# Kernel optimization log

Hardware: AMD Instinct MI355X
Metric: run time of the kernel (lower is better)

## Reference

```python
import jax, jax.numpy as jnp
import numpy as np

EMBED_DIM = 256
NUM_CLASSES = 10


def setup_inputs() -> dict:
    key = jax.random.key(0)
    k1, k2, k3, k4 = jax.random.split(key, 4)
    x = jax.random.normal(k1, (64, 196, 768), dtype=jnp.float32)
    ag_w = jax.random.normal(k2, (EMBED_DIM, 768), dtype=jnp.float32)
    ag_b = jax.random.normal(k3, (EMBED_DIM,), dtype=jnp.float32)
    lm_w = jax.random.normal(k4, (EMBED_DIM * NUM_CLASSES, 768), dtype=jnp.float32)
    return {"x": x, "ag_w": ag_w, "ag_b": ag_b, "lm_w": lm_w}


def reference(x, ag_w, ag_b, lm_w):
    # x: (B, HW, D); ag_w: (E, D); ag_b: (E,); lm_w: (E*C, D)
    B, HW, D = x.shape
    E, C = EMBED_DIM, NUM_CLASSES
    # frozen arrangement generator -> binary sign pattern (B, HW, E)
    sign_patterns = (jnp.einsum('bhd,ed->bhe', x, ag_w) + ag_b > 0).astype(x.dtype)
    # linear map: (B, HW, E*C) -> (B, HW, E, C)
    z = jnp.einsum('bhd,pd->bhp', x, lm_w).reshape(B, HW, E, C)
    # masked reduction over HW and embed dims
    preds = jnp.einsum('bhp,bhpc->bc', sign_patterns, z) / HW
    return preds / E
```

## Files before the change

### kernel.cpp

```cpp
#include <hip/hip_runtime.h>

#define B_    64
#define HW_   196
#define HWP_  224
#define D_    768
#define E_    256
#define C_    10
#define MP_   (B_*HWP_)
#define K3K_  (E_*D_)
#define K3NB_ 192

typedef __bf16 bf16x8 __attribute__((ext_vector_type(8)));
typedef __bf16 bf16x4 __attribute__((ext_vector_type(4)));
typedef float  f32x4  __attribute__((ext_vector_type(4)));

__device__ __forceinline__ void gld_lds16(const void* g, void* l) {
  __builtin_amdgcn_global_load_lds((const __attribute__((address_space(1))) void*)g,
                                   (__attribute__((address_space(3))) void*)l, 16, 0, 0);
}

__global__ __launch_bounds__(256) void k0_x(const float* __restrict__ x,
                                            __bf16* __restrict__ xhi,
                                            __bf16* __restrict__ xlo) {
  size_t i4 = ((size_t)blockIdx.x * 256 + threadIdx.x) * 4;
  int d  = (int)(i4 % D_);
  size_t row = i4 / D_;
  int hp = (int)(row % HWP_);
  int b  = (int)(row / HWP_);
  float4 v = make_float4(0.f, 0.f, 0.f, 0.f);
  if (hp < HW_) v = *(const float4*)&x[((size_t)b * HW_ + hp) * D_ + d];
  float vv[4] = {v.x, v.y, v.z, v.w};
  bf16x4 h, l;
#pragma unroll
  for (int j = 0; j < 4; j++) {
    __bf16 hj = (__bf16)vv[j];
    float r = vv[j] - (float)hj;
    h[j] = hj;
    l[j] = (__bf16)r;
  }
  *(bf16x4*)&xhi[i4] = h;
  *(bf16x4*)&xlo[i4] = l;
}

__global__ __launch_bounds__(256) void k0_prep(const float* __restrict__ w,
                                               __bf16* __restrict__ whi,
                                               __bf16* __restrict__ wlo,
                                               const float* __restrict__ lmw,
                                               __bf16* __restrict__ w2) {
  int bid = blockIdx.x;
  if (bid < 192) {
    size_t i4 = ((size_t)bid * 256 + threadIdx.x) * 4;
    float4 v = *(const float4*)&w[i4];
    float vv[4] = {v.x, v.y, v.z, v.w};
    bf16x4 h, l;
#pragma unroll
    for (int j = 0; j < 4; j++) {
      __bf16 hj = (__bf16)vv[j];
      float r = vv[j] - (float)hj;
      h[j] = hj;
      l[j] = (__bf16)r;
    }
    *(bf16x4*)&whi[i4] = h;
    *(bf16x4*)&wlo[i4] = l;
  } else {
    size_t i4 = ((size_t)(bid - 192) * 256 + threadIdx.x) * 4;
    int c = (int)(i4 / K3K_);
    int rem = (int)(i4 - (size_t)c * K3K_);
    int e = rem / D_;
    int d = rem - e * D_;
    bf16x4 o;
    if (c < C_) {
      float4 v = *(const float4*)&lmw[((size_t)e * C_ + c) * D_ + d];
      o[0] = (__bf16)v.x; o[1] = (__bf16)v.y; o[2] = (__bf16)v.z; o[3] = (__bf16)v.w;
    } else {
      o[0] = o[1] = o[2] = o[3] = (__bf16)0.0f;
    }
    *(bf16x4*)&w2[i4] = o;
  }
}

__global__ __launch_bounds__(256) void k1_signs(const __bf16* __restrict__ xhi,
                                                const __bf16* __restrict__ xlo,
                                                const __bf16* __restrict__ whi,
                                                const __bf16* __restrict__ wlo,
                                                const float* __restrict__ bias,
                                                __bf16* __restrict__ st) {
  __shared__ __align__(16) __bf16 Ah[2][64 * 32];
  __shared__ __align__(16) __bf16 Al[2][64 * 32];
  __shared__ __align__(16) __bf16 Bh[2][64 * 32];
  __shared__ __align__(16) __bf16 Bl[2][64 * 32];
  const int m0 = blockIdx.x * 64;
  const int n0 = blockIdx.y * 64;
  const int tid = threadIdx.x;
  const int wave = tid >> 6, lane = tid & 63;
  const int wm = (wave & 1) * 32, wn = (wave >> 1) * 32;
  const int q = lane >> 4, l15 = lane & 15;
  const int sr = tid >> 2;
  const int sk = (tid & 3) * 8;
  const int ldsoff = wave * 512;
  f32x4 acc[2][2] = {};

  const __bf16* gAh = &xhi[(size_t)(m0 + sr) * D_ + sk];
  const __bf16* gAl = &xlo[(size_t)(m0 + sr) * D_ + sk];
  const __bf16* gBh = &whi[(size_t)(n0 + sr) * D_ + sk];
  const __bf16* gBl = &wlo[(size_t)(n0 + sr) * D_ + sk];

  gld_lds16(gAh, &Ah[0][ldsoff]);
  gld_lds16(gAl, &Al[0][ldsoff]);
  gld_lds16(gBh, &Bh[0][ldsoff]);
  gld_lds16(gBl, &Bl[0][ldsoff]);
  __syncthreads();

  int cur = 0;
  for (int k0 = 0; k0 < D_; k0 += 32) {
    if (k0 + 32 < D_) {
      gld_lds16(gAh + k0 + 32, &Ah[cur ^ 1][ldsoff]);
      gld_lds16(gAl + k0 + 32, &Al[cur ^ 1][ldsoff]);
      gld_lds16(gBh + k0 + 32, &Bh[cur ^ 1][ldsoff]);
      gld_lds16(gBl + k0 + 32, &Bl[cur ^ 1][ldsoff]);
    }
    bf16x8 af[2], alf[2], bfh[2], bfl[2];
#pragma unroll
    for (int t = 0; t < 2; t++) {
      af[t]  = *(const bf16x8*)&Ah[cur][(wm + t * 16 + l15) * 32 + q * 8];
      alf[t] = *(const bf16x8*)&Al[cur][(wm + t * 16 + l15) * 32 + q * 8];
      bfh[t] = *(const bf16x8*)&Bh[cur][(wn + t * 16 + l15) * 32 + q * 8];
      bfl[t] = *(const bf16x8*)&Bl[cur][(wn + t * 16 + l15) * 32 + q * 8];
    }
#pragma unroll
    for (int mt = 0; mt < 2; mt++)
#pragma unroll
      for (int nt = 0; nt < 2; nt++) {
        acc[mt][nt] = __builtin_amdgcn_mfma_f32_16x16x32_bf16(af[mt],  bfh[nt], acc[mt][nt], 0, 0, 0);
        acc[mt][nt] = __builtin_amdgcn_mfma_f32_16x16x32_bf16(alf[mt], bfh[nt], acc[mt][nt], 0, 0, 0);
        acc[mt][nt] = __builtin_amdgcn_mfma_f32_16x16x32_bf16(af[mt],  bfl[nt], acc[mt][nt], 0, 0, 0);
      }
    __syncthreads();
    cur ^= 1;
  }
#pragma unroll
  for (int mt = 0; mt < 2; mt++)
#pragma unroll
    for (int nt = 0; nt < 2; nt++) {
      int e = n0 + wn + nt * 16 + l15;
      float bv = bias[e];
#pragma unroll
      for (int r = 0; r < 4; r++) {
        int m = m0 + wm + mt * 16 + q * 4 + r;
        int b = m / HWP_;
        int hp = m - b * HWP_;
        float v = acc[mt][nt][r] + bv;
        __bf16 s = (hp < HW_ && v > 0.0f) ? (__bf16)1.0f : (__bf16)0.0f;
        st[((size_t)b * E_ + e) * HWP_ + hp] = s;
      }
    }
}

__global__ __launch_bounds__(256) void k2_g(const __bf16* __restrict__ st,
                                            const __bf16* __restrict__ xhi,
                                            __bf16* __restrict__ g) {
  __shared__ __align__(16) __bf16 As[2][128 * 32];
  __shared__ __align__(16) __bf16 Bs[2][128 * 40];
  const int b  = blockIdx.y;
  const int e0 = (blockIdx.x / 6) * 128;
  const int d0 = (blockIdx.x % 6) * 128;
  const int tid = threadIdx.x;
  const int wave = tid >> 6, lane = tid & 63;
  const int wm = (wave & 1) * 64, wn = (wave >> 1) * 64;
  const int q = lane >> 4, l15 = lane & 15;
  const int sr = tid >> 2, sk = (tid & 3) * 8;
  const int ldsoff = wave * 512;
  const int kk4 = ((tid >> 2) & 7) * 4;
  const int dgroup = (tid & 3) | (((tid >> 5) & 7) << 2);
  const int dc0 = dgroup * 4;
  f32x4 acc[4][4] = {};

  const __bf16* gA0 = &st[((size_t)b * E_ + e0 + sr) * HWP_ + sk];
  const __bf16* gA1 = &st[((size_t)b * E_ + e0 + 64 + sr) * HWP_ + sk];
  const __bf16* gB  = &xhi[((size_t)b * HWP_ + kk4) * D_ + d0 + dc0];

  gld_lds16(gA0, &As[0][ldsoff]);
  gld_lds16(gA1, &As[0][64 * 32 + ldsoff]);
  {
    bf16x4 r0 = *(const bf16x4*)&gB[0];
    bf16x4 r1 = *(const bf16x4*)&gB[D_];
    bf16x4 r2 = *(const bf16x4*)&gB[2 * D_];
    bf16x4 r3 = *(const bf16x4*)&gB[3 * D_];
#pragma unroll
    for (int j = 0; j < 4; j++) {
      bf16x4 o;
      o[0] = r0[j]; o[1] = r1[j]; o[2] = r2[j]; o[3] = r3[j];
      *(bf16x4*)&Bs[0][(dc0 + j) * 40 + kk4] = o;
    }
  }
  __syncthreads();

  int cur = 0;
  for (int k0 = 0; k0 < HWP_; k0 += 32) {
    const bool have = (k0 + 32 < HWP_);
    bf16x4 r0, r1, r2, r3;
    if (have) {
      gld_lds16(gA0 + k0 + 32, &As[cur ^ 1][ldsoff]);
      gld_lds16(gA1 + k0 + 32, &As[cur ^ 1][64 * 32 + ldsoff]);
      const __bf16* src = gB + (size_t)(k0 + 32) * D_;
      r0 = *(const bf16x4*)&src[0];
      r1 = *(const bf16x4*)&src[D_];
      r2 = *(const bf16x4*)&src[2 * D_];
      r3 = *(const bf16x4*)&src[3 * D_];
    }
    bf16x8 af[4], bfr[4];
#pragma unroll
    for (int t = 0; t < 4; t++) {
      af[t]  = *(const bf16x8*)&As[cur][(wm + t * 16 + l15) * 32 + q * 8];
      bfr[t] = *(const bf16x8*)&Bs[cur][(wn + t * 16 + l15) * 40 + q * 8];
    }
#pragma unroll
    for (int mt = 0; mt < 4; mt++)
#pragma unroll
      for (int nt = 0; nt < 4; nt++)
        acc[mt][nt] = __builtin_amdgcn_mfma_f32_16x16x32_bf16(af[mt], bfr[nt], acc[mt][nt], 0, 0, 0);
    if (have) {
#pragma unroll
      for (int j = 0; j < 4; j++) {
        bf16x4 o;
        o[0] = r0[j]; o[1] = r1[j]; o[2] = r2[j]; o[3] = r3[j];
        *(bf16x4*)&Bs[cur ^ 1][(dc0 + j) * 40 + kk4] = o;
      }
    }
    __syncthreads();
    cur ^= 1;
  }
#pragma unroll
  for (int mt = 0; mt < 4; mt++)
#pragma unroll
    for (int nt = 0; nt < 4; nt++) {
      int d = d0 + wn + nt * 16 + l15;
#pragma unroll
      for (int r = 0; r < 4; r++) {
        int e = e0 + wm + mt * 16 + q * 4 + r;
        g[((size_t)b * E_ + e) * D_ + d] = (__bf16)acc[mt][nt][r];
      }
    }
}

__global__ __launch_bounds__(256) void k3_mfma(const __bf16* __restrict__ g,
                                               const __bf16* __restrict__ w2,
                                               float* __restrict__ out) {
  __shared__ float sp[B_ * C_];
  const int tid = threadIdx.x;
  const int wave = tid >> 6, lane = tid & 63;
  const int q = lane >> 4, l15 = lane & 15;
  const int kbase = blockIdx.x * (K3K_ / K3NB_) + wave * 256;
  f32x4 acc[4] = {};

  for (int i = tid; i < B_ * C_; i += 256) sp[i] = 0.0f;

#pragma unroll
  for (int ks = 0; ks < 8; ks++) {
    int k = kbase + ks * 32 + q * 8;
    bf16x8 bfrag = *(const bf16x8*)&w2[(size_t)l15 * K3K_ + k];
#pragma unroll
    for (int mt = 0; mt < 4; mt++) {
      bf16x8 afrag = *(const bf16x8*)&g[(size_t)(mt * 16 + l15) * K3K_ + k];
      acc[mt] = __builtin_amdgcn_mfma_f32_16x16x32_bf16(afrag, bfrag, acc[mt], 0, 0, 0);
    }
  }
  __syncthreads();
  int c = l15;
  if (c < C_) {
#pragma unroll
    for (int mt = 0; mt < 4; mt++)
#pragma unroll
      for (int r = 0; r < 4; r++) {
        int b = mt * 16 + q * 4 + r;
        atomicAdd(&sp[b * C_ + c], acc[mt][r]);
      }
  }
  __syncthreads();
  const float scale = 1.0f / (196.0f * 256.0f);
  for (int i = tid; i < B_ * C_; i += 256) atomicAdd(&out[i], sp[i] * scale);
}

extern "C" void kernel_launch(void* const* d_in, const int* in_sizes, int n_in,
                              void* d_out, int out_size, void* d_ws, size_t ws_size,
                              hipStream_t stream) {
  const float* x    = (const float*)d_in[0];
  const float* ag_w = (const float*)d_in[1];
  const float* ag_b = (const float*)d_in[2];
  const float* lm_w = (const float*)d_in[3];
  float* out = (float*)d_out;

  char* ws = (char*)d_ws;
  const size_t XP_BYTES = (size_t)B_ * HWP_ * D_ * 2;
  const size_t W_BYTES  = (size_t)E_ * D_ * 2;
  const size_t ST_BYTES = (size_t)B_ * E_ * HWP_ * 2;
  const size_t G_BYTES  = (size_t)B_ * E_ * D_ * 2;
  __bf16* xhi = (__bf16*)(ws);
  __bf16* xlo = (__bf16*)(ws + XP_BYTES);
  __bf16* whi = (__bf16*)(ws + 2 * XP_BYTES);
  __bf16* wlo = (__bf16*)(ws + 2 * XP_BYTES + W_BYTES);
  __bf16* st  = (__bf16*)(ws + 2 * XP_BYTES + 2 * W_BYTES);
  __bf16* gb  = (__bf16*)(ws + 2 * XP_BYTES + 2 * W_BYTES + ST_BYTES);
  __bf16* w2  = (__bf16*)(ws + 2 * XP_BYTES + 2 * W_BYTES + ST_BYTES + G_BYTES);

  hipMemsetAsync(d_out, 0, (size_t)out_size * sizeof(float), stream);

  k0_x<<<dim3((B_ * HWP_ * D_) / 4 / 256), dim3(256), 0, stream>>>(x, xhi, xlo);
  k0_prep<<<dim3(192 + (16 * K3K_) / 4 / 256), dim3(256), 0, stream>>>(ag_w, whi, wlo, lm_w, w2);
  k1_signs<<<dim3(MP_ / 64, E_ / 64), dim3(256), 0, stream>>>(xhi, xlo, whi, wlo, ag_b, st);
  k2_g<<<dim3((E_ / 128) * (D_ / 128), B_), dim3(256), 0, stream>>>(st, xhi, gb);
  k3_mfma<<<dim3(K3NB_), dim3(256), 0, stream>>>(gb, w2, out);
}
```

Measured before the change: 163.3 us.

## Enlarge k1 tiles to 128x128, swizzle LDS layouts, split k3 across more blocks

The sign GEMM kernel moves from 64x64 to 128x128 tiles with a 4x4 MFMA grid per wave. This raises arithmetic intensity and cuts redundant global loads of the hi/lo operands. LDS rows in k1 and the A tile in k2 use an XOR swizzle of the 16-byte chunk index to reduce bank conflicts on the fragment reads. The final reduction kernel doubles its block count, halving the K range per block, to expose more parallelism at the cost of more atomics. The larger k1 tile raises register and LDS pressure and halves the grid, which may lower occupancy.

After: 168.3 us. 1.03x slower.

```diff
diff --git a/kernel.cpp b/kernel.cpp
--- a/kernel.cpp
+++ b/kernel.cpp
@@ -8,7 +8,7 @@
 #define C_    10
 #define MP_   (B_*HWP_)
 #define K3K_  (E_*D_)
-#define K3NB_ 192
+#define K3NB_ 384
 
 typedef __bf16 bf16x8 __attribute__((ext_vector_type(8)));
 typedef __bf16 bf16x4 __attribute__((ext_vector_type(4)));
@@ -85,63 +85,71 @@
                                                 const __bf16* __restrict__ wlo,
                                                 const float* __restrict__ bias,
                                                 __bf16* __restrict__ st) {
-  __shared__ __align__(16) __bf16 Ah[2][64 * 32];
-  __shared__ __align__(16) __bf16 Al[2][64 * 32];
-  __shared__ __align__(16) __bf16 Bh[2][64 * 32];
-  __shared__ __align__(16) __bf16 Bl[2][64 * 32];
-  const int m0 = blockIdx.x * 64;
-  const int n0 = blockIdx.y * 64;
+  __shared__ __align__(16) __bf16 Ah[2][128 * 32];
+  __shared__ __align__(16) __bf16 Al[2][128 * 32];
+  __shared__ __align__(16) __bf16 Bh[2][128 * 32];
+  __shared__ __align__(16) __bf16 Bl[2][128 * 32];
+  const int m0 = blockIdx.x * 128;
+  const int n0 = blockIdx.y * 128;
   const int tid = threadIdx.x;
   const int wave = tid >> 6, lane = tid & 63;
-  const int wm = (wave & 1) * 32, wn = (wave >> 1) * 32;
+  const int wm = (wave & 1) * 64, wn = (wave >> 1) * 64;
   const int q = lane >> 4, l15 = lane & 15;
-  const int sr = tid >> 2;
-  const int sk = (tid & 3) * 8;
-  const int ldsoff = wave * 512;
-  f32x4 acc[2][2] = {};
-
-  const __bf16* gAh = &xhi[(size_t)(m0 + sr) * D_ + sk];
-  const __bf16* gAl = &xlo[(size_t)(m0 + sr) * D_ + sk];
-  const __bf16* gBh = &whi[(size_t)(n0 + sr) * D_ + sk];
-  const __bf16* gBl = &wlo[(size_t)(n0 + sr) * D_ + sk];
-
-  gld_lds16(gAh, &Ah[0][ldsoff]);
-  gld_lds16(gAl, &Al[0][ldsoff]);
-  gld_lds16(gBh, &Bh[0][ldsoff]);
-  gld_lds16(gBl, &Bl[0][ldsoff]);
+  const int r0 = wave * 32 + (lane >> 2);
+  const int sc = ((lane & 3) ^ ((r0 >> 1) & 3)) * 8;
+  const int ld0 = wave * 32 * 32;
+  const int ld1 = ld0 + 16 * 32;
+  const size_t offA = (size_t)(m0 + r0) * D_ + sc;
+  const size_t offB = (size_t)(n0 + r0) * D_ + sc;
+  const size_t rstep = (size_t)16 * D_;
+  f32x4 acc[4][4] = {};
+
+#define K1_STAGE(buf, kk) do { \
+    gld_lds16(&xhi[offA + (kk)],         &Ah[buf][ld0]); \
+    gld_lds16(&xhi[offA + rstep + (kk)], &Ah[buf][ld1]); \
+    gld_lds16(&xlo[offA + (kk)],         &Al[buf][ld0]); \
+    gld_lds16(&xlo[offA + rstep + (kk)], &Al[buf][ld1]); \
+    gld_lds16(&whi[offB + (kk)],         &Bh[buf][ld0]); \
+    gld_lds16(&whi[offB + rstep + (kk)], &Bh[buf][ld1]); \
+    gld_lds16(&wlo[offB + (kk)],         &Bl[buf][ld0]); \
+    gld_lds16(&wlo[offB + rstep + (kk)], &Bl[buf][ld1]); \
+  } while (0)
+
+  K1_STAGE(0, 0);
   __syncthreads();
 
   int cur = 0;
   for (int k0 = 0; k0 < D_; k0 += 32) {
-    if (k0 + 32 < D_) {
-      gld_lds16(gAh + k0 + 32, &Ah[cur ^ 1][ldsoff]);
-      gld_lds16(gAl + k0 + 32, &Al[cur ^ 1][ldsoff]);
-      gld_lds16(gBh + k0 + 32, &Bh[cur ^ 1][ldsoff]);
-      gld_lds16(gBl + k0 + 32, &Bl[cur ^ 1][ldsoff]);
-    }
-    bf16x8 af[2], alf[2], bfh[2], bfl[2];
-#pragma unroll
-    for (int t = 0; t < 2; t++) {
-      af[t]  = *(const bf16x8*)&Ah[cur][(wm + t * 16 + l15) * 32 + q * 8];
-      alf[t] = *(const bf16x8*)&Al[cur][(wm + t * 16 + l15) * 32 + q * 8];
-      bfh[t] = *(const bf16x8*)&Bh[cur][(wn + t * 16 + l15) * 32 + q * 8];
-      bfl[t] = *(const bf16x8*)&Bl[cur][(wn + t * 16 + l15) * 32 + q * 8];
-    }
-#pragma unroll
-    for (int mt = 0; mt < 2; mt++)
-#pragma unroll
-      for (int nt = 0; nt < 2; nt++) {
-        acc[mt][nt] = __builtin_amdgcn_mfma_f32_16x16x32_bf16(af[mt],  bfh[nt], acc[mt][nt], 0, 0, 0);
-        acc[mt][nt] = __builtin_amdgcn_mfma_f32_16x16x32_bf16(alf[mt], bfh[nt], acc[mt][nt], 0, 0, 0);
-        acc[mt][nt] = __builtin_amdgcn_mfma_f32_16x16x32_bf16(af[mt],  bfl[nt], acc[mt][nt], 0, 0, 0);
+    if (k0 + 32 < D_) K1_STAGE(cur ^ 1, k0 + 32);
+    bf16x8 ah[4], al[4], bh[4], bl[4];
+#pragma unroll
+    for (int t = 0; t < 4; t++) {
+      int ra = wm + t * 16 + l15;
+      int rb = wn + t * 16 + l15;
+      int sa = (q ^ ((ra >> 1) & 3)) * 8;
+      int sb = (q ^ ((rb >> 1) & 3)) * 8;
+      ah[t] = *(const bf16x8*)&Ah[cur][ra * 32 + sa];
+      al[t] = *(const bf16x8*)&Al[cur][ra * 32 + sa];
+      bh[t] = *(const bf16x8*)&Bh[cur][rb * 32 + sb];
+      bl[t] = *(const bf16x8*)&Bl[cur][rb * 32 + sb];
+    }
+#pragma unroll
+    for (int mt = 0; mt < 4; mt++)
+#pragma unroll
+      for (int nt = 0; nt < 4; nt++) {
+        acc[mt][nt] = __builtin_amdgcn_mfma_f32_16x16x32_bf16(ah[mt], bh[nt], acc[mt][nt], 0, 0, 0);
+        acc[mt][nt] = __builtin_amdgcn_mfma_f32_16x16x32_bf16(al[mt], bh[nt], acc[mt][nt], 0, 0, 0);
+        acc[mt][nt] = __builtin_amdgcn_mfma_f32_16x16x32_bf16(ah[mt], bl[nt], acc[mt][nt], 0, 0, 0);
       }
     __syncthreads();
     cur ^= 1;
   }
-#pragma unroll
-  for (int mt = 0; mt < 2; mt++)
-#pragma unroll
-    for (int nt = 0; nt < 2; nt++) {
+#undef K1_STAGE
+
+#pragma unroll
+  for (int mt = 0; mt < 4; mt++)
+#pragma unroll
+    for (int nt = 0; nt < 4; nt++) {
       int e = n0 + wn + nt * 16 + l15;
       float bv = bias[e];
 #pragma unroll
@@ -168,15 +176,16 @@
   const int wave = tid >> 6, lane = tid & 63;
   const int wm = (wave & 1) * 64, wn = (wave >> 1) * 64;
   const int q = lane >> 4, l15 = lane & 15;
-  const int sr = tid >> 2, sk = (tid & 3) * 8;
+  const int sr = tid >> 2;
+  const int scA = ((lane & 3) ^ ((sr >> 1) & 3)) * 8;
   const int ldsoff = wave * 512;
   const int kk4 = ((tid >> 2) & 7) * 4;
   const int dgroup = (tid & 3) | (((tid >> 5) & 7) << 2);
   const int dc0 = dgroup * 4;
   f32x4 acc[4][4] = {};
 
-  const __bf16* gA0 = &st[((size_t)b * E_ + e0 + sr) * HWP_ + sk];
-  const __bf16* gA1 = &st[((size_t)b * E_ + e0 + 64 + sr) * HWP_ + sk];
+  const __bf16* gA0 = &st[((size_t)b * E_ + e0 + sr) * HWP_ + scA];
+  const __bf16* gA1 = gA0 + (size_t)64 * HWP_;
   const __bf16* gB  = &xhi[((size_t)b * HWP_ + kk4) * D_ + d0 + dc0];
 
   gld_lds16(gA0, &As[0][ldsoff]);
@@ -211,7 +220,9 @@
     bf16x8 af[4], bfr[4];
 #pragma unroll
     for (int t = 0; t < 4; t++) {
-      af[t]  = *(const bf16x8*)&As[cur][(wm + t * 16 + l15) * 32 + q * 8];
+      int ra = wm + t * 16 + l15;
+      int sa = (q ^ ((ra >> 1) & 3)) * 8;
+      af[t]  = *(const bf16x8*)&As[cur][ra * 32 + sa];
       bfr[t] = *(const bf16x8*)&Bs[cur][(wn + t * 16 + l15) * 40 + q * 8];
     }
 #pragma unroll
@@ -250,13 +261,13 @@
   const int tid = threadIdx.x;
   const int wave = tid >> 6, lane = tid & 63;
   const int q = lane >> 4, l15 = lane & 15;
-  const int kbase = blockIdx.x * (K3K_ / K3NB_) + wave * 256;
+  const int kbase = blockIdx.x * (K3K_ / K3NB_) + wave * 128;
   f32x4 acc[4] = {};
 
   for (int i = tid; i < B_ * C_; i += 256) sp[i] = 0.0f;
 
 #pragma unroll
-  for (int ks = 0; ks < 8; ks++) {
+  for (int ks = 0; ks < 4; ks++) {
     int k = kbase + ks * 32 + q * 8;
     bf16x8 bfrag = *(const bf16x8*)&w2[(size_t)l15 * K3K_ + k];
 #pragma unroll
@@ -307,7 +318,7 @@
 
   k0_x<<<dim3((B_ * HWP_ * D_) / 4 / 256), dim3(256), 0, stream>>>(x, xhi, xlo);
   k0_prep<<<dim3(192 + (16 * K3K_) / 4 / 256), dim3(256), 0, stream>>>(ag_w, whi, wlo, lm_w, w2);
-  k1_signs<<<dim3(MP_ / 64, E_ / 64), dim3(256), 0, stream>>>(xhi, xlo, whi, wlo, ag_b, st);
+  k1_signs<<<dim3(MP_ / 128, E_ / 128), dim3(256), 0, stream>>>(xhi, xlo, whi, wlo, ag_b, st);
   k2_g<<<dim3((E_ / 128) * (D_ / 128), B_), dim3(256), 0, stream>>>(st, xhi, gb);
   k3_mfma<<<dim3(K3NB_), dim3(256), 0, stream>>>(gb, w2, out);
 }
```
